# Optimization experiments

Measured on AMD Instinct MI355X. Metric: run time of the kernel, lower is better.

The kernel has to match this reference:

```python
import jax, jax.numpy as jnp
import numpy as np

H = 1024   # hidden_size
V = 32000  # output_size (vocab)
L = 3      # num_decoder_layers
B = 64     # batch
T = 32     # max_length


def setup_inputs() -> dict:
    key = jax.random.key(0)
    ks = jax.random.split(key, 10)
    s = 1.0 / np.sqrt(H)
    u = lambda k, shape: jax.random.uniform(k, shape, jnp.float32, -s, s)
    return {
        "encoder_outputs": jax.random.normal(ks[0], (B, T, H), jnp.float32),
        "encoder_hidden": jax.random.normal(ks[1], (L, B, H), jnp.float32),
        "target_tensor": jax.random.randint(ks[2], (B, T), 0, V),
        "emb": u(ks[3], (V, H)),
        "W_ih": u(ks[4], (L, 3 * H, H)),
        "W_hh": u(ks[5], (L, 3 * H, H)),
        "b_ih": u(ks[6], (L, 3 * H)),
        "b_hh": u(ks[7], (L, 3 * H)),
        "W_out": u(ks[8], (V, H)),
        "b_out": u(ks[9], (V,)),
    }


def _gru_layer(x, h0, Wih, Whh, bih, bhh):
    # x: [B,T,H], h0: [B,H]; PyTorch GRU gate order: r, z, n
    xp = jnp.einsum('bth,gh->btg', x, Wih) + bih  # [B,T,3H], input projections hoisted out of scan

    def step(h, xpt):
        hp = h @ Whh.T + bhh  # [B,3H]
        r = jax.nn.sigmoid(xpt[:, :H] + hp[:, :H])
        z = jax.nn.sigmoid(xpt[:, H:2 * H] + hp[:, H:2 * H])
        n = jnp.tanh(xpt[:, 2 * H:] + r * hp[:, 2 * H:])
        hn = (1.0 - z) * n + z * h
        return hn, hn

    hT, ys = jax.lax.scan(step, h0, jnp.swapaxes(xp, 0, 1))  # time-major scan
    return jnp.swapaxes(ys, 0, 1), hT  # [B,T,H], [B,H]


def reference(encoder_outputs, encoder_hidden, target_tensor, emb, W_ih, W_hh, b_ih, b_hh, W_out, b_out):
    # Teacher forcing: step 0 consumes SOS token 0, step i consumes target[:, i-1]
    ids = jnp.concatenate([jnp.zeros((B, 1), target_tensor.dtype), target_tensor[:, :-1]], axis=1)  # [B,T]
    x = jax.nn.relu(emb[ids])  # [B,T,H]
    finals = []
    for l in range(L):  # small fixed layer loop
        x, hT = _gru_layer(x, encoder_hidden[l], W_ih[l], W_hh[l], b_ih[l], b_hh[l])
        finals.append(hT)
    logits = jnp.einsum('bth,vh->btv', x, W_out) + b_out  # [B,T,V]
    log_probs = jax.nn.log_softmax(logits, axis=-1)
    return log_probs, jnp.stack(finals, axis=0)
```

## Files before the change

kernel.cpp:

```cpp
#include <hip/hip_runtime.h>
#include <hip/hip_bf16.h>
#include <cstdint>
#include <cstddef>

#define Hdim 1024
#define Vdim 32000
#define LAYERS 3
#define Bdim 64
#define Tdim 32
#define BT 2048
#define G3H 3072

using bf16 = __bf16;
using bf16x8 = __attribute__((ext_vector_type(8))) __bf16;
using bf16x4 = __attribute__((ext_vector_type(4))) __bf16;
using f32x4  = __attribute__((ext_vector_type(4))) float;

typedef const __attribute__((address_space(1))) void* gas1_t;
typedef __attribute__((address_space(3))) void* las3_t;
__device__ __forceinline__ void g2lds16(const void* g, void* l) {
  __builtin_amdgcn_global_load_lds((gas1_t)g, (las3_t)l, 16, 0, 0);
}

__global__ __launch_bounds__(256) void cvt_f32_bf16(const float* __restrict__ src,
                                                    bf16* __restrict__ dst, int n4) {
  int i = blockIdx.x * 256 + threadIdx.x;
  if (i < n4) {
    f32x4 v = ((const f32x4*)src)[i];
    bf16x4 o;
    o[0] = (bf16)v[0]; o[1] = (bf16)v[1]; o[2] = (bf16)v[2]; o[3] = (bf16)v[3];
    ((bf16x4*)dst)[i] = o;
  }
}

__global__ __launch_bounds__(256) void embed_relu(const int* __restrict__ tgt,
                                                  const float* __restrict__ emb,
                                                  bf16* __restrict__ x) {
  int row = blockIdx.x;
  int b = row >> 5, t = row & 31;
  int id = (t == 0) ? 0 : tgt[b * Tdim + t - 1];
  const f32x4* src = (const f32x4*)(emb + (size_t)id * Hdim);
  bf16x4* dst = (bf16x4*)(x + (size_t)row * Hdim);
  f32x4 v = src[threadIdx.x];
  bf16x4 o;
  o[0] = (bf16)fmaxf(v[0], 0.f); o[1] = (bf16)fmaxf(v[1], 0.f);
  o[2] = (bf16)fmaxf(v[2], 0.f); o[3] = (bf16)fmaxf(v[3], 0.f);
  dst[threadIdx.x] = o;
}

__global__ __launch_bounds__(256) void hinit(const float* __restrict__ eh,
                                             float* __restrict__ h32,
                                             bf16* __restrict__ hbf) {
  int i = blockIdx.x * 256 + threadIdx.x;
  f32x4 v = ((const f32x4*)eh)[i];
  ((f32x4*)h32)[i] = v;
  bf16x4 o;
  o[0] = (bf16)v[0]; o[1] = (bf16)v[1]; o[2] = (bf16)v[2]; o[3] = (bf16)v[3];
  ((bf16x4*)hbf)[i] = o;
}

template <bool BIAS>
__global__ __launch_bounds__(256) void gemm_lds(const bf16* __restrict__ A,
                                                const bf16* __restrict__ Bm,
                                                const float* __restrict__ bias,
                                                float* __restrict__ C,
                                                int M, int N, int K) {
  __shared__ bf16 As[128 * 32];
  __shared__ bf16 Bs[128 * 32];

  int wave = threadIdx.x >> 6, lane = threadIdx.x & 63;
  int lane15 = lane & 15, quad = lane >> 4;
  int wr = wave >> 1, wc = wave & 1;
  int m0 = blockIdx.x * 128;
  int n0 = blockIdx.y * 128;

  int srow = wave * 16 + (lane >> 2);
  int scol = (lane & 3) * 8;
  const bf16* Asrc = A + (size_t)(m0 + srow) * K + scol;
  const bf16* Bsrc = Bm + (size_t)(n0 + srow) * K + scol;
  bf16* AdstW = As + (size_t)wave * 512;
  bf16* BdstW = Bs + (size_t)wave * 512;

  f32x4 acc[4][4] = {};
  for (int k0 = 0; k0 < K; k0 += 32) {
#pragma unroll
    for (int r = 0; r < 2; r++) {
      g2lds16(Asrc + (size_t)(r * 64) * K + k0, AdstW + r * 2048);
      g2lds16(Bsrc + (size_t)(r * 64) * K + k0, BdstW + r * 2048);
    }
    __syncthreads();

    bf16x8 a[4], b[4];
#pragma unroll
    for (int mi = 0; mi < 4; mi++)
      a[mi] = *(const bf16x8*)&As[(wr * 64 + mi * 16 + lane15) * 32 + quad * 8];
#pragma unroll
    for (int ni = 0; ni < 4; ni++)
      b[ni] = *(const bf16x8*)&Bs[(wc * 64 + ni * 16 + lane15) * 32 + quad * 8];
#pragma unroll
    for (int mi = 0; mi < 4; mi++)
#pragma unroll
      for (int ni = 0; ni < 4; ni++)
        acc[mi][ni] = __builtin_amdgcn_mfma_f32_16x16x32_bf16(a[mi], b[ni], acc[mi][ni], 0, 0, 0);
    __syncthreads();
  }

#pragma unroll
  for (int mi = 0; mi < 4; mi++)
#pragma unroll
    for (int ni = 0; ni < 4; ni++) {
      int col = n0 + wc * 64 + ni * 16 + lane15;
      float bv = BIAS ? bias[col] : 0.f;
#pragma unroll
      for (int r = 0; r < 4; r++) {
        int row = m0 + wr * 64 + mi * 16 + quad * 4 + r;
        C[(size_t)row * N + col] = acc[mi][ni][r] + bv;
      }
    }
}

__global__ __launch_bounds__(256) void gru_step(const bf16* __restrict__ hbf_p,
                                                const float* __restrict__ h32_p,
                                                const bf16* __restrict__ Whh,
                                                const float* __restrict__ bhh,
                                                const float* __restrict__ xp,
                                                float* __restrict__ h32_n,
                                                bf16* __restrict__ hbf_n,
                                                bf16* __restrict__ y,
                                                float* __restrict__ finals,
                                                int t) {
  __shared__ float part[3][4][256];
  int tid = threadIdx.x;
  int wave = tid >> 6, lane = tid & 63;
  int lane15 = lane & 15, quad = lane >> 4;
  int i0 = blockIdx.x * 16, b0 = blockIdx.y * 16;
  int kbase = wave * 256;

  const bf16* Ap = hbf_p + (size_t)(b0 + lane15) * Hdim + kbase + quad * 8;
  const bf16* Br = Whh + (size_t)(0 * Hdim + i0 + lane15) * Hdim + kbase + quad * 8;
  const bf16* Bz = Whh + (size_t)(1 * Hdim + i0 + lane15) * Hdim + kbase + quad * 8;
  const bf16* Bn = Whh + (size_t)(2 * Hdim + i0 + lane15) * Hdim + kbase + quad * 8;

  f32x4 ar = {}, az = {}, an = {};
#pragma unroll
  for (int k0 = 0; k0 < 256; k0 += 32) {
    bf16x8 a  = *(const bf16x8*)(Ap + k0);
    bf16x8 br = *(const bf16x8*)(Br + k0);
    bf16x8 bz = *(const bf16x8*)(Bz + k0);
    bf16x8 bn = *(const bf16x8*)(Bn + k0);
    ar = __builtin_amdgcn_mfma_f32_16x16x32_bf16(a, br, ar, 0, 0, 0);
    az = __builtin_amdgcn_mfma_f32_16x16x32_bf16(a, bz, az, 0, 0, 0);
    an = __builtin_amdgcn_mfma_f32_16x16x32_bf16(a, bn, an, 0, 0, 0);
  }
#pragma unroll
  for (int r = 0; r < 4; r++) {
    int idx = (quad * 4 + r) * 16 + lane15;
    part[0][wave][idx] = ar[r];
    part[1][wave][idx] = az[r];
    part[2][wave][idx] = an[r];
  }
  __syncthreads();

  int b_local = tid >> 4, i_local = tid & 15;
  float hr = part[0][0][tid] + part[0][1][tid] + part[0][2][tid] + part[0][3][tid];
  float hz = part[1][0][tid] + part[1][1][tid] + part[1][2][tid] + part[1][3][tid];
  float hn = part[2][0][tid] + part[2][1][tid] + part[2][2][tid] + part[2][3][tid];
  int i = i0 + i_local, b = b0 + b_local;
  hr += bhh[i]; hz += bhh[Hdim + i]; hn += bhh[2 * Hdim + i];
  size_t m = (size_t)b * Tdim + t;
  float xr = xp[m * G3H + i];
  float xz = xp[m * G3H + Hdim + i];
  float xn = xp[m * G3H + 2 * Hdim + i];
  float rg = 1.f / (1.f + __expf(-(xr + hr)));
  float zg = 1.f / (1.f + __expf(-(xz + hz)));
  float ng = tanhf(xn + rg * hn);
  float hold = h32_p[(size_t)b * Hdim + i];
  float hnew = (1.f - zg) * ng + zg * hold;
  h32_n[(size_t)b * Hdim + i] = hnew;
  hbf_n[(size_t)b * Hdim + i] = (bf16)hnew;
  y[m * Hdim + i] = (bf16)hnew;
  if (t == Tdim - 1) finals[(size_t)b * Hdim + i] = hnew;
}

__global__ __launch_bounds__(256) void logsoftmax(float* __restrict__ out) {
  __shared__ float sm[256], ss[256];
  int row = blockIdx.x;
  f32x4* x = (f32x4*)(out + (size_t)row * Vdim);
  const int n4 = Vdim / 4;
  float m = -1e30f, s = 0.f;
  for (int j = threadIdx.x; j < n4; j += 256) {
    f32x4 v = x[j];
    float vm = fmaxf(fmaxf(v[0], v[1]), fmaxf(v[2], v[3]));
    float nm = fmaxf(m, vm);
    s = s * __expf(m - nm) + __expf(v[0] - nm) + __expf(v[1] - nm)
                           + __expf(v[2] - nm) + __expf(v[3] - nm);
    m = nm;
  }
  sm[threadIdx.x] = m; ss[threadIdx.x] = s;
  __syncthreads();
  for (int off = 128; off; off >>= 1) {
    if (threadIdx.x < off) {
      float m1 = sm[threadIdx.x], s1 = ss[threadIdx.x];
      float m2 = sm[threadIdx.x + off], s2 = ss[threadIdx.x + off];
      float mm = fmaxf(m1, m2);
      sm[threadIdx.x] = mm;
      ss[threadIdx.x] = s1 * __expf(m1 - mm) + s2 * __expf(m2 - mm);
    }
    __syncthreads();
  }
  float lse = sm[0] + logf(ss[0]);
  for (int j = threadIdx.x; j < n4; j += 256) {
    f32x4 v = x[j];
    v[0] -= lse; v[1] -= lse; v[2] -= lse; v[3] -= lse;
    x[j] = v;
  }
}

extern "C" void kernel_launch(void* const* d_in, const int* in_sizes, int n_in,
                              void* d_out, int out_size, void* d_ws, size_t ws_size,
                              hipStream_t stream) {
  const float* enc_hidden = (const float*)d_in[1];
  const int*   target     = (const int*)d_in[2];
  const float* emb        = (const float*)d_in[3];
  const float* W_ih       = (const float*)d_in[4];
  const float* W_hh       = (const float*)d_in[5];
  const float* b_ih       = (const float*)d_in[6];
  const float* b_hh       = (const float*)d_in[7];
  const float* W_out      = (const float*)d_in[8];
  const float* b_out      = (const float*)d_in[9];

  float* out = (float*)d_out;
  float* finals = out + (size_t)BT * Vdim;

  uint8_t* wsp = (uint8_t*)d_ws;
  auto alloc = [&](size_t bytes) {
    uint8_t* p = wsp;
    wsp += (bytes + 255) & ~(size_t)255;
    return p;
  };
  bf16* wih_bf  = (bf16*)alloc((size_t)LAYERS * G3H * Hdim * 2);
  bf16* whh_bf  = (bf16*)alloc((size_t)LAYERS * G3H * Hdim * 2);
  bf16* wout_bf = (bf16*)alloc((size_t)Vdim * Hdim * 2);
  bf16* xA      = (bf16*)alloc((size_t)BT * Hdim * 2);
  bf16* xB      = (bf16*)alloc((size_t)BT * Hdim * 2);
  float* xp     = (float*)alloc((size_t)BT * G3H * 4);
  float* h32a   = (float*)alloc((size_t)Bdim * Hdim * 4);
  float* h32b   = (float*)alloc((size_t)Bdim * Hdim * 4);
  bf16* hbfa    = (bf16*)alloc((size_t)Bdim * Hdim * 2);
  bf16* hbfb    = (bf16*)alloc((size_t)Bdim * Hdim * 2);
  float* h32[2] = {h32a, h32b};
  bf16*  hbf[2] = {hbfa, hbfb};

  {
    int n4 = LAYERS * G3H * Hdim / 4;
    cvt_f32_bf16<<<(n4 + 255) / 256, 256, 0, stream>>>(W_ih, wih_bf, n4);
    cvt_f32_bf16<<<(n4 + 255) / 256, 256, 0, stream>>>(W_hh, whh_bf, n4);
    int m4 = Vdim * Hdim / 4;
    cvt_f32_bf16<<<(m4 + 255) / 256, 256, 0, stream>>>(W_out, wout_bf, m4);
  }

  embed_relu<<<BT, 256, 0, stream>>>(target, emb, xA);

  bf16* xin = xA;
  bf16* xout_ = xB;
  for (int l = 0; l < LAYERS; l++) {
    hinit<<<64, 256, 0, stream>>>(enc_hidden + (size_t)l * Bdim * Hdim, h32[0], hbf[0]);
    dim3 g1(BT / 128, G3H / 128);
    gemm_lds<true><<<g1, 256, 0, stream>>>(xin, wih_bf + (size_t)l * G3H * Hdim,
                                           b_ih + (size_t)l * G3H, xp, BT, G3H, Hdim);
    for (int t = 0; t < Tdim; t++) {
      int p = t & 1;
      gru_step<<<dim3(Hdim / 16, Bdim / 16), 256, 0, stream>>>(
          hbf[p], h32[p], whh_bf + (size_t)l * G3H * Hdim, b_hh + (size_t)l * G3H,
          xp, h32[p ^ 1], hbf[p ^ 1], xout_, finals + (size_t)l * Bdim * Hdim, t);
    }
    bf16* tmp = xin; xin = xout_; xout_ = tmp;
  }

  dim3 g2(BT / 128, Vdim / 128);
  gemm_lds<true><<<g2, 256, 0, stream>>>(xin, wout_bf, b_out, out, BT, Vdim, Hdim);

  logsoftmax<<<BT, 256, 0, stream>>>(out);
}
```

Before: 1.526 ms.

## Fuse GRU timesteps into one persistent kernel with grid barrier and register-resident weights

Replaces the 32 per-timestep gru_step launches per layer with a single persistent 256-block kernel. Each block keeps its slice of W_hh in registers and carries the fp32 hidden state in a register, and a global atomic counter acts as a grid-wide barrier between timesteps. This removes repeated launch overhead and the per-step reloads of W_hh and of the fp32 hidden state. It also remaps GEMM tile indices so consecutive blocks spread across the 8 XCDs. The spin barrier relies on all 256 blocks being co-resident, and the inline atomic wait adds latency to every step.

```diff
diff --git a/kernel.cpp b/kernel.cpp
--- a/kernel.cpp
+++ b/kernel.cpp
@@ -49,11 +49,11 @@
 }
 
 __global__ __launch_bounds__(256) void hinit(const float* __restrict__ eh,
-                                             float* __restrict__ h32,
-                                             bf16* __restrict__ hbf) {
+                                             bf16* __restrict__ hbf,
+                                             unsigned int* __restrict__ ctr) {
+  if (blockIdx.x == 0 && threadIdx.x == 0) *ctr = 0u;
   int i = blockIdx.x * 256 + threadIdx.x;
   f32x4 v = ((const f32x4*)eh)[i];
-  ((f32x4*)h32)[i] = v;
   bf16x4 o;
   o[0] = (bf16)v[0]; o[1] = (bf16)v[1]; o[2] = (bf16)v[2]; o[3] = (bf16)v[3];
   ((bf16x4*)hbf)[i] = o;
@@ -71,8 +71,14 @@
   int wave = threadIdx.x >> 6, lane = threadIdx.x & 63;
   int lane15 = lane & 15, quad = lane >> 4;
   int wr = wave >> 1, wc = wave & 1;
-  int m0 = blockIdx.x * 128;
-  int n0 = blockIdx.y * 128;
+
+  int flat = blockIdx.y * gridDim.x + blockIdx.x;
+  int per = (gridDim.x * gridDim.y) >> 3;
+  int nid = (flat & 7) * per + (flat >> 3);
+  int mt = nid % gridDim.x;
+  int nt = nid / gridDim.x;
+  int m0 = mt * 128;
+  int n0 = nt * 128;
 
   int srow = wave * 16 + (lane >> 2);
   int scol = (lane & 3) * 8;
@@ -119,67 +125,97 @@
     }
 }
 
-__global__ __launch_bounds__(256) void gru_step(const bf16* __restrict__ hbf_p,
-                                                const float* __restrict__ h32_p,
-                                                const bf16* __restrict__ Whh,
-                                                const float* __restrict__ bhh,
-                                                const float* __restrict__ xp,
-                                                float* __restrict__ h32_n,
-                                                bf16* __restrict__ hbf_n,
-                                                bf16* __restrict__ y,
-                                                float* __restrict__ finals,
-                                                int t) {
+__global__ __launch_bounds__(256, 1) void gru_layer(
+    const bf16* __restrict__ hbf0,
+    const float* __restrict__ eh,
+    const bf16* __restrict__ Whh,
+    const float* __restrict__ bhh,
+    const float* __restrict__ xp,
+    bf16* __restrict__ hbfa,
+    bf16* __restrict__ hbfb,
+    bf16* __restrict__ y,
+    float* __restrict__ finals,
+    unsigned int* __restrict__ ctr) {
   __shared__ float part[3][4][256];
   int tid = threadIdx.x;
   int wave = tid >> 6, lane = tid & 63;
   int lane15 = lane & 15, quad = lane >> 4;
-  int i0 = blockIdx.x * 16, b0 = blockIdx.y * 16;
+  int bid = blockIdx.x;
+  int i0 = (bid & 63) * 16;
+  int b0 = (bid >> 6) * 16;
   int kbase = wave * 256;
 
-  const bf16* Ap = hbf_p + (size_t)(b0 + lane15) * Hdim + kbase + quad * 8;
-  const bf16* Br = Whh + (size_t)(0 * Hdim + i0 + lane15) * Hdim + kbase + quad * 8;
-  const bf16* Bz = Whh + (size_t)(1 * Hdim + i0 + lane15) * Hdim + kbase + quad * 8;
-  const bf16* Bn = Whh + (size_t)(2 * Hdim + i0 + lane15) * Hdim + kbase + quad * 8;
-
-  f32x4 ar = {}, az = {}, an = {};
-#pragma unroll
-  for (int k0 = 0; k0 < 256; k0 += 32) {
-    bf16x8 a  = *(const bf16x8*)(Ap + k0);
-    bf16x8 br = *(const bf16x8*)(Br + k0);
-    bf16x8 bz = *(const bf16x8*)(Bz + k0);
-    bf16x8 bn = *(const bf16x8*)(Bn + k0);
-    ar = __builtin_amdgcn_mfma_f32_16x16x32_bf16(a, br, ar, 0, 0, 0);
-    az = __builtin_amdgcn_mfma_f32_16x16x32_bf16(a, bz, az, 0, 0, 0);
-    an = __builtin_amdgcn_mfma_f32_16x16x32_bf16(a, bn, an, 0, 0, 0);
-  }
-#pragma unroll
-  for (int r = 0; r < 4; r++) {
-    int idx = (quad * 4 + r) * 16 + lane15;
-    part[0][wave][idx] = ar[r];
-    part[1][wave][idx] = az[r];
-    part[2][wave][idx] = an[r];
-  }
-  __syncthreads();
+  const bf16* Wr = Whh + (size_t)(i0 + lane15) * Hdim + kbase + quad * 8;
+  const bf16* Wz = Wr + (size_t)Hdim * Hdim;
+  const bf16* Wn = Wr + 2 * (size_t)Hdim * Hdim;
+  bf16x8 wr_[8], wz_[8], wn_[8];
+#pragma unroll
+  for (int j = 0; j < 8; j++) {
+    wr_[j] = *(const bf16x8*)(Wr + j * 32);
+    wz_[j] = *(const bf16x8*)(Wz + j * 32);
+    wn_[j] = *(const bf16x8*)(Wn + j * 32);
+  }
 
   int b_local = tid >> 4, i_local = tid & 15;
-  float hr = part[0][0][tid] + part[0][1][tid] + part[0][2][tid] + part[0][3][tid];
-  float hz = part[1][0][tid] + part[1][1][tid] + part[1][2][tid] + part[1][3][tid];
-  float hn = part[2][0][tid] + part[2][1][tid] + part[2][2][tid] + part[2][3][tid];
-  int i = i0 + i_local, b = b0 + b_local;
-  hr += bhh[i]; hz += bhh[Hdim + i]; hn += bhh[2 * Hdim + i];
-  size_t m = (size_t)b * Tdim + t;
-  float xr = xp[m * G3H + i];
-  float xz = xp[m * G3H + Hdim + i];
-  float xn = xp[m * G3H + 2 * Hdim + i];
-  float rg = 1.f / (1.f + __expf(-(xr + hr)));
-  float zg = 1.f / (1.f + __expf(-(xz + hz)));
-  float ng = tanhf(xn + rg * hn);
-  float hold = h32_p[(size_t)b * Hdim + i];
-  float hnew = (1.f - zg) * ng + zg * hold;
-  h32_n[(size_t)b * Hdim + i] = hnew;
-  hbf_n[(size_t)b * Hdim + i] = (bf16)hnew;
-  y[m * Hdim + i] = (bf16)hnew;
-  if (t == Tdim - 1) finals[(size_t)b * Hdim + i] = hnew;
+  int i_out = i0 + i_local;
+  int b_out = b0 + b_local;
+  float bhr = bhh[i_out], bhz = bhh[Hdim + i_out], bhn = bhh[2 * Hdim + i_out];
+  size_t hi = (size_t)b_out * Hdim + i_out;
+  float hold = eh[hi];
+  const float* xpr = xp + ((size_t)b_out * Tdim) * G3H;
+
+  unsigned int target = 0;
+  for (int t = 0; t < Tdim; t++) {
+    const bf16* hp = (t & 1) ? hbfb : hbfa;
+    bf16*       hn_ = (t & 1) ? hbfa : hbfb;
+
+    float xr = xpr[(size_t)t * G3H + i_out];
+    float xz = xpr[(size_t)t * G3H + Hdim + i_out];
+    float xn = xpr[(size_t)t * G3H + 2 * Hdim + i_out];
+
+    const bf16* Ap = hp + (size_t)(b0 + lane15) * Hdim + kbase + quad * 8;
+    bf16x8 a[8];
+#pragma unroll
+    for (int j = 0; j < 8; j++) a[j] = *(const bf16x8*)(Ap + j * 32);
+    f32x4 ar = {}, az = {}, an = {};
+#pragma unroll
+    for (int j = 0; j < 8; j++) {
+      ar = __builtin_amdgcn_mfma_f32_16x16x32_bf16(a[j], wr_[j], ar, 0, 0, 0);
+      az = __builtin_amdgcn_mfma_f32_16x16x32_bf16(a[j], wz_[j], az, 0, 0, 0);
+      an = __builtin_amdgcn_mfma_f32_16x16x32_bf16(a[j], wn_[j], an, 0, 0, 0);
+    }
+#pragma unroll
+    for (int r = 0; r < 4; r++) {
+      int idx = (quad * 4 + r) * 16 + lane15;
+      part[0][wave][idx] = ar[r];
+      part[1][wave][idx] = az[r];
+      part[2][wave][idx] = an[r];
+    }
+    __syncthreads();
+
+    float hr = part[0][0][tid] + part[0][1][tid] + part[0][2][tid] + part[0][3][tid] + bhr;
+    float hz = part[1][0][tid] + part[1][1][tid] + part[1][2][tid] + part[1][3][tid] + bhz;
+    float hnp = part[2][0][tid] + part[2][1][tid] + part[2][2][tid] + part[2][3][tid] + bhn;
+    float rg = 1.f / (1.f + __expf(-(xr + hr)));
+    float zg = 1.f / (1.f + __expf(-(xz + hz)));
+    float ng = tanhf(xn + rg * hnp);
+    float hnew = (1.f - zg) * ng + zg * hold;
+    hold = hnew;
+    hn_[hi] = (bf16)hnew;
+    y[((size_t)b_out * Tdim + t) * Hdim + i_out] = (bf16)hnew;
+
+    __syncthreads();
+    __threadfence();
+    target += 256;
+    if (tid == 0) {
+      __hip_atomic_fetch_add(ctr, 1u, __ATOMIC_RELEASE, __HIP_MEMORY_SCOPE_AGENT);
+      while (__hip_atomic_load(ctr, __ATOMIC_RELAXED, __HIP_MEMORY_SCOPE_AGENT) < target)
+        __builtin_amdgcn_s_sleep(2);
+    }
+    __syncthreads();
+    __threadfence();
+  }
+  finals[hi] = hold;
 }
 
 __global__ __launch_bounds__(256) void logsoftmax(float* __restrict__ out) {
@@ -244,12 +280,9 @@
   bf16* xA      = (bf16*)alloc((size_t)BT * Hdim * 2);
   bf16* xB      = (bf16*)alloc((size_t)BT * Hdim * 2);
   float* xp     = (float*)alloc((size_t)BT * G3H * 4);
-  float* h32a   = (float*)alloc((size_t)Bdim * Hdim * 4);
-  float* h32b   = (float*)alloc((size_t)Bdim * Hdim * 4);
   bf16* hbfa    = (bf16*)alloc((size_t)Bdim * Hdim * 2);
   bf16* hbfb    = (bf16*)alloc((size_t)Bdim * Hdim * 2);
-  float* h32[2] = {h32a, h32b};
-  bf16*  hbf[2] = {hbfa, hbfb};
+  unsigned int* ctr = (unsigned int*)alloc(256);
 
   {
     int n4 = LAYERS * G3H * Hdim / 4;
@@ -264,16 +297,16 @@
   bf16* xin = xA;
   bf16* xout_ = xB;
   for (int l = 0; l < LAYERS; l++) {
-    hinit<<<64, 256, 0, stream>>>(enc_hidden + (size_t)l * Bdim * Hdim, h32[0], hbf[0]);
+    const float* eh_l = enc_hidden + (size_t)l * Bdim * Hdim;
+    hinit<<<64, 256, 0, stream>>>(eh_l, hbfa, ctr);
     dim3 g1(BT / 128, G3H / 128);
     gemm_lds<true><<<g1, 256, 0, stream>>>(xin, wih_bf + (size_t)l * G3H * Hdim,
                                            b_ih + (size_t)l * G3H, xp, BT, G3H, Hdim);
-    for (int t = 0; t < Tdim; t++) {
-      int p = t & 1;
-      gru_step<<<dim3(Hdim / 16, Bdim / 16), 256, 0, stream>>>(
-          hbf[p], h32[p], whh_bf + (size_t)l * G3H * Hdim, b_hh + (size_t)l * G3H,
-          xp, h32[p ^ 1], hbf[p ^ 1], xout_, finals + (size_t)l * Bdim * Hdim, t);
-    }
+    gru_layer<<<256, 256, 0, stream>>>(hbfa, eh_l,
+                                       whh_bf + (size_t)l * G3H * Hdim,
+                                       b_hh + (size_t)l * G3H, xp,
+                                       hbfa, hbfb, xout_,
+                                       finals + (size_t)l * Bdim * Hdim, ctr);
     bf16* tmp = xin; xin = xout_; xout_ = tmp;
   }
 
```

Measured after the change: 5.496 ms. 260% more time.
